# Kernel tuning notes

Measured on AMD Instinct MI355X. Metric: run time of the kernel, lower is better.

## Reference

```python
import jax, jax.numpy as jnp
import numpy as np

# --- constants matching ElectrostaticEnergy defaults ---
KE = 14.399645351950548
KEHALF = KE / 2.0
CUTON = 2.5
CUTOFF = 7.5
LR_CUTOFF = 10.0
CUTON16 = CUTON ** 16
CUT_RCONSTANT = LR_CUTOFF ** 15 / (LR_CUTOFF ** 16 + CUTON ** 16) ** (17.0 / 16.0)
CUT_CONSTANT = 1.0 / (CUTON ** 16 + LR_CUTOFF ** 16) ** (1.0 / 16.0) + LR_CUTOFF ** 16 / (LR_CUTOFF ** 16 + CUTON ** 16) ** (17.0 / 16.0)

N_ATOMS = 102400   # total atoms
N_PAIRS = N_ATOMS * 64  # 6,553,600 edges
N_MOL = 2048       # molecules (atoms per molecule = 50)


def switch_function(x):
    """SpookyNet-style smooth switch: 1 below cuton, 0 above cutoff."""
    t = (CUTOFF - x) / (CUTOFF - CUTON)

    def comp(u):
        u_safe = jnp.where(u <= 0, jnp.ones_like(u), u)
        return jnp.where(u <= 0, jnp.zeros_like(u), jnp.exp(-1.0 / u_safe))

    fp = comp(t)
    fm = comp(1.0 - t)
    return jnp.where(t <= 0, jnp.zeros_like(t),
                     jnp.where(t >= 1, jnp.ones_like(t), fp / (fp + fm)))


def setup_inputs() -> dict:
    key = jax.random.key(0)
    k1, k2, k3, k4, k5 = jax.random.split(key, 5)
    atomic_numbers = jax.random.randint(k1, (N_ATOMS,), 1, 10, dtype=jnp.int32)
    q = 0.1 * jax.random.normal(k2, (N_ATOMS,), dtype=jnp.float32)  # partial charges
    # uniform components in [0.8, 6.5] -> d_ij roughly in [1.4, 11.2], spans all cutoffs
    r_ij = jax.random.uniform(k3, (N_PAIRS, 3), dtype=jnp.float32, minval=0.8, maxval=6.5)
    idx_i = jax.random.randint(k4, (N_PAIRS,), 0, N_ATOMS, dtype=jnp.int32)
    idx_j = jax.random.randint(k5, (N_PAIRS,), 0, N_ATOMS, dtype=jnp.int32)
    idx_m = jnp.repeat(jnp.arange(N_MOL, dtype=jnp.int32), N_ATOMS // N_MOL)  # sorted atom->mol map
    return {"atomic_numbers": atomic_numbers, "q": q, "r_ij": r_ij,
            "idx_i": idx_i, "idx_j": idx_j, "idx_m": idx_m, "maxm": N_MOL}


def reference(atomic_numbers, q, r_ij, idx_i, idx_j, idx_m, maxm):
    N = q.shape[0]
    d_ij = jnp.linalg.norm(r_ij, axis=1)                      # [P]
    fac = KEHALF * q[idx_i] * q[idx_j]                        # [P] gather
    f = switch_function(d_ij)                                 # [P]
    # lr_cutoff branch of the original module
    x_coulomb = 1.0 / d_ij + d_ij / (LR_CUTOFF ** 2) - 2.0 / LR_CUTOFF
    coulomb = jnp.where(d_ij < LR_CUTOFF, x_coulomb, jnp.zeros_like(d_ij))
    damped = (d_ij ** 16 + CUTON16) ** (-1.0 / 16.0) + (1.0 - f) * CUT_RCONSTANT * d_ij - CUT_CONSTANT
    e_edge = fac * (f * damped + (1.0 - f) * coulomb)         # [P]
    y_atom = jax.ops.segment_sum(e_edge, idx_i, num_segments=N)        # edge -> atom
    y = jax.ops.segment_sum(y_atom, idx_m, num_segments=maxm)          # atom -> molecule
    return y  # [maxm]
```

## Files before the change

kernel.cpp:

```cpp
#include <hip/hip_runtime.h>
#include <math.h>

#define NMOL  2048
#define APM   50u
#define BLOCK 512
#define GRID  512

__global__ void zero_y_kernel(float* __restrict__ y, int n) {
    int i = blockIdx.x * blockDim.x + threadIdx.x;
    if (i < n) y[i] = 0.0f;
}

__launch_bounds__(BLOCK, 4)
__global__ void edge_energy_kernel(const float* __restrict__ q,
                                   const float* __restrict__ r,
                                   const int*   __restrict__ idx_i,
                                   const int*   __restrict__ idx_j,
                                   float*       __restrict__ y,
                                   int P)
{
    __shared__ float bins[NMOL];
    for (int b = threadIdx.x; b < NMOL; b += BLOCK) bins[b] = 0.0f;
    __syncthreads();

    const float KEHALF_F   = 7.199822675975274f;
    const float CUTOFF_F   = 7.5f;
    const float INV_RANGE  = 0.2f;
    const float LRC        = 10.0f;
    const float CUTON16_F  = 2328306.4365386963f;
    const float CUT_RCONST = 0.009999999997526949f;
    const float CUT_CONST  = 0.19999999997381023f;

    const int stride = GRID * BLOCK;
    for (int p = blockIdx.x * BLOCK + threadIdx.x; p < P; p += stride) {
        const float x  = r[3 * p + 0];
        const float yv = r[3 * p + 1];
        const float z  = r[3 * p + 2];
        const int   i  = idx_i[p];
        const int   j  = idx_j[p];

        const float d   = sqrtf(fmaf(x, x, fmaf(yv, yv, z * z)));
        const float fac = KEHALF_F * q[i] * q[j];

        const float t = (CUTOFF_F - d) * INV_RANGE;
        float f;
        if (t <= 0.0f) {
            f = 0.0f;
        } else if (t >= 1.0f) {
            f = 1.0f;
        } else {
            const float fp = __expf(-__builtin_amdgcn_rcpf(t));
            const float fm = __expf(-__builtin_amdgcn_rcpf(1.0f - t));
            f = fp * __builtin_amdgcn_rcpf(fp + fm);
        }

        const float invd = __builtin_amdgcn_rcpf(d);
        const float coul = (d < LRC) ? (invd + d * 0.01f - 0.2f) : 0.0f;

        const float d2 = d * d, d4 = d2 * d2, d8 = d4 * d4, d16 = d8 * d8;
        const float damped = __expf(-0.0625f * __logf(d16 + CUTON16_F))
                           + (1.0f - f) * CUT_RCONST * d - CUT_CONST;

        const float e = fac * (f * damped + (1.0f - f) * coul);

        const int mol = (int)((unsigned)i / APM);
        atomicAdd(&bins[mol], e);
    }

    __syncthreads();
    const int off = (blockIdx.x * 97) & (NMOL - 1);
    for (int b0 = threadIdx.x; b0 < NMOL; b0 += BLOCK) {
        const int b = (b0 + off) & (NMOL - 1);
        const float v = bins[b];
        if (v != 0.0f) unsafeAtomicAdd(&y[b], v);
    }
}

extern "C" void kernel_launch(void* const* d_in, const int* in_sizes, int n_in,
                              void* d_out, int out_size, void* d_ws, size_t ws_size,
                              hipStream_t stream) {
    const float* q     = (const float*)d_in[1];
    const float* r_ij  = (const float*)d_in[2];
    const int*   idx_i = (const int*)d_in[3];
    const int*   idx_j = (const int*)d_in[4];
    float*       y     = (float*)d_out;
    const int P = in_sizes[3];

    zero_y_kernel<<<(out_size + 255) / 256, 256, 0, stream>>>(y, out_size);
    edge_energy_kernel<<<GRID, BLOCK, 0, stream>>>(q, r_ij, idx_i, idx_j, y, P);
}
```

Before: 224.7 us.

## Process four edges per thread with vectorized loads and branchless switch

Each thread now handles groups of four edges, loading coordinates as three float4 and the indices as int4. This gives wide coalesced loads and exposes more independent gathers per thread. The switch function is made branchless by clamping t, so the exp/rcp work is always computed in place of divergent branches. Block size doubles to 1024, and the flush drops the zero check on bins. The change trades more registers per thread for fewer memory instructions, which could limit occupancy.

```diff
diff --git a/kernel.cpp b/kernel.cpp
--- a/kernel.cpp
+++ b/kernel.cpp
@@ -3,7 +3,7 @@
 
 #define NMOL  2048
 #define APM   50u
-#define BLOCK 512
+#define BLOCK 1024
 #define GRID  512
 
 __global__ void zero_y_kernel(float* __restrict__ y, int n) {
@@ -11,7 +11,32 @@
     if (i < n) y[i] = 0.0f;
 }
 
-__launch_bounds__(BLOCK, 4)
+#define KEHALF_F   7.199822675975274f
+#define CUTON16_F  2328306.4365386963f
+#define CUT_RCONST 0.01f
+#define CUT_CONST  0.2f
+
+__device__ __forceinline__ float edge_energy(float x, float yv, float z,
+                                             float qi, float qj) {
+    const float d   = sqrtf(fmaf(x, x, fmaf(yv, yv, z * z)));
+    const float fac = KEHALF_F * qi * qj;
+
+    const float t  = fminf(fmaxf((7.5f - d) * 0.2f, 0.0f), 1.0f);
+    const float fp = __expf(-__builtin_amdgcn_rcpf(t));
+    const float fm = __expf(-__builtin_amdgcn_rcpf(1.0f - t));
+    const float f  = fp * __builtin_amdgcn_rcpf(fp + fm);
+
+    const float invd = __builtin_amdgcn_rcpf(d);
+    const float coul = (d < 10.0f) ? fmaf(d, 0.01f, invd - 0.2f) : 0.0f;
+
+    const float d2 = d * d, d4 = d2 * d2, d8 = d4 * d4, d16 = d8 * d8;
+    const float damped = __expf(-0.0625f * __logf(d16 + CUTON16_F))
+                       + (1.0f - f) * (CUT_RCONST * d) - CUT_CONST;
+
+    return fac * (f * damped + (1.0f - f) * coul);
+}
+
+__launch_bounds__(BLOCK, 8)
 __global__ void edge_energy_kernel(const float* __restrict__ q,
                                    const float* __restrict__ r,
                                    const int*   __restrict__ idx_i,
@@ -23,56 +48,47 @@
     for (int b = threadIdx.x; b < NMOL; b += BLOCK) bins[b] = 0.0f;
     __syncthreads();
 
-    const float KEHALF_F   = 7.199822675975274f;
-    const float CUTOFF_F   = 7.5f;
-    const float INV_RANGE  = 0.2f;
-    const float LRC        = 10.0f;
-    const float CUTON16_F  = 2328306.4365386963f;
-    const float CUT_RCONST = 0.009999999997526949f;
-    const float CUT_CONST  = 0.19999999997381023f;
+    const int ngroups = P >> 2;
+    const int stride  = GRID * BLOCK;
+    const float4* r4   = (const float4*)r;
+    const int4*   i4p  = (const int4*)idx_i;
+    const int4*   j4p  = (const int4*)idx_j;
 
-    const int stride = GRID * BLOCK;
-    for (int p = blockIdx.x * BLOCK + threadIdx.x; p < P; p += stride) {
-        const float x  = r[3 * p + 0];
-        const float yv = r[3 * p + 1];
-        const float z  = r[3 * p + 2];
-        const int   i  = idx_i[p];
-        const int   j  = idx_j[p];
+    for (int g = blockIdx.x * BLOCK + threadIdx.x; g < ngroups; g += stride) {
+        const float4 ra = r4[3 * g + 0];
+        const float4 rb = r4[3 * g + 1];
+        const float4 rc = r4[3 * g + 2];
+        const int4   ii = i4p[g];
+        const int4   jj = j4p[g];
 
-        const float d   = sqrtf(fmaf(x, x, fmaf(yv, yv, z * z)));
-        const float fac = KEHALF_F * q[i] * q[j];
+        const float qi0 = q[ii.x], qj0 = q[jj.x];
+        const float qi1 = q[ii.y], qj1 = q[jj.y];
+        const float qi2 = q[ii.z], qj2 = q[jj.z];
+        const float qi3 = q[ii.w], qj3 = q[jj.w];
 
-        const float t = (CUTOFF_F - d) * INV_RANGE;
-        float f;
-        if (t <= 0.0f) {
-            f = 0.0f;
-        } else if (t >= 1.0f) {
-            f = 1.0f;
-        } else {
-            const float fp = __expf(-__builtin_amdgcn_rcpf(t));
-            const float fm = __expf(-__builtin_amdgcn_rcpf(1.0f - t));
-            f = fp * __builtin_amdgcn_rcpf(fp + fm);
-        }
+        const float e0 = edge_energy(ra.x, ra.y, ra.z, qi0, qj0);
+        const float e1 = edge_energy(ra.w, rb.x, rb.y, qi1, qj1);
+        const float e2 = edge_energy(rb.z, rb.w, rc.x, qi2, qj2);
+        const float e3 = edge_energy(rc.y, rc.z, rc.w, qi3, qj3);
 
-        const float invd = __builtin_amdgcn_rcpf(d);
-        const float coul = (d < LRC) ? (invd + d * 0.01f - 0.2f) : 0.0f;
+        atomicAdd(&bins[(unsigned)ii.x / APM], e0);
+        atomicAdd(&bins[(unsigned)ii.y / APM], e1);
+        atomicAdd(&bins[(unsigned)ii.z / APM], e2);
+        atomicAdd(&bins[(unsigned)ii.w / APM], e3);
+    }
 
-        const float d2 = d * d, d4 = d2 * d2, d8 = d4 * d4, d16 = d8 * d8;
-        const float damped = __expf(-0.0625f * __logf(d16 + CUTON16_F))
-                           + (1.0f - f) * CUT_RCONST * d - CUT_CONST;
-
-        const float e = fac * (f * damped + (1.0f - f) * coul);
-
-        const int mol = (int)((unsigned)i / APM);
-        atomicAdd(&bins[mol], e);
+    for (int p = (ngroups << 2) + blockIdx.x * BLOCK + threadIdx.x; p < P;
+         p += stride) {
+        const float e = edge_energy(r[3 * p], r[3 * p + 1], r[3 * p + 2],
+                                    q[idx_i[p]], q[idx_j[p]]);
+        atomicAdd(&bins[(unsigned)idx_i[p] / APM], e);
     }
 
     __syncthreads();
     const int off = (blockIdx.x * 97) & (NMOL - 1);
     for (int b0 = threadIdx.x; b0 < NMOL; b0 += BLOCK) {
         const int b = (b0 + off) & (NMOL - 1);
-        const float v = bins[b];
-        if (v != 0.0f) unsafeAtomicAdd(&y[b], v);
+        unsafeAtomicAdd(&y[b], bins[b]);
     }
 }
 
```

Result: faster. 214.4 us (-4.6%).
